# Performance work log

Hardware: AMD Instinct MI355X
Metric: run time of the kernel (lower is better)

Reference implementation:

```python
import jax, jax.numpy as jnp
import numpy as np

N_NODES = 32768
N_EDGES = 131072
B = 1024          # number of drug graphs
N_SIDE = 994      # SIDER side effects
SIDE_F = 1050     # glove(300) + label(750)

GAT_DIMS = [(109, 96, 8), (768, 128, 8), (1024, 128, 8), (1024, 128, 1)]  # (in, out_per_head, heads)
LIN_DIMS = [("x5", 128, 64), ("x6", 64, 64), ("w1", 750, 750), ("w2", 750, 64),
            ("z1", 19127, 1600), ("z2", 1600, 64), ("v1", 1024, 256), ("v2", 256, 64),
            ("agg", 192, 64), ("col", 128, 64), ("s1", SIDE_F, 64), ("s2", 64, 64)]


def setup_inputs() -> dict:
    key = jax.random.key(0)
    ks = iter(jax.random.split(key, 64))
    d = {}
    d["x"] = jax.random.normal(next(ks), (N_NODES, 109), jnp.float32)
    d["edge_index"] = jax.random.randint(next(ks), (2, N_EDGES), 0, N_NODES)
    d["batch"] = jnp.arange(N_NODES) // (N_NODES // B)  # 32 atoms per graph
    d["w"] = jax.random.normal(next(ks), (B, 750), jnp.float32)
    d["z"] = jax.random.normal(next(ks), (B, 19127), jnp.float32)
    d["v"] = jax.random.normal(next(ks), (B, 1024), jnp.float32)
    d["side"] = jax.random.normal(next(ks), (N_SIDE, SIDE_F), jnp.float32)
    for i, (fi, fo, h) in enumerate(GAT_DIMS, 1):
        d[f"g{i}_W"] = jax.random.normal(next(ks), (fi, h * fo), jnp.float32) / np.sqrt(fi)
        d[f"g{i}_as"] = jax.random.normal(next(ks), (1, h, fo), jnp.float32) * 0.1
        d[f"g{i}_ad"] = jax.random.normal(next(ks), (1, h, fo), jnp.float32) * 0.1
        d[f"g{i}_b"] = jnp.zeros((h * fo,), jnp.float32)
    for name, fi, fo in LIN_DIMS:
        d[name + "_W"] = jax.random.normal(next(ks), (fi, fo), jnp.float32) / np.sqrt(fi)
        d[name + "_b"] = jnp.zeros((fo,), jnp.float32)
    return d


def _gat(x, src, dst, W, a_s, a_d, b, heads, ch):
    """PyG GATConv (eval mode): linear -> per-edge leaky_relu attention ->
    scatter-softmax over incoming edges (self-loops already in src/dst) -> scatter-sum."""
    N = x.shape[0]
    h = (x @ W).reshape(N, heads, ch)            # [N,H,C]
    al_s = (h * a_s).sum(-1)                     # [N,H]
    al_d = (h * a_d).sum(-1)                     # [N,H]
    e = jax.nn.leaky_relu(al_s[src] + al_d[dst], 0.2)  # [E,H]
    m = jax.ops.segment_max(e, dst, num_segments=N)
    p = jnp.exp(e - m[dst])
    s = jax.ops.segment_sum(p, dst, num_segments=N)
    alpha = p / s[dst]                           # softmax over neighbors of dst
    out = jax.ops.segment_sum(h[src] * alpha[:, :, None], dst, num_segments=N)
    return out.reshape(N, heads * ch) + b


def reference(x, edge_index, batch, w, z, v, side,
              g1_W, g1_as, g1_ad, g1_b, g2_W, g2_as, g2_ad, g2_b,
              g3_W, g3_as, g3_ad, g3_b, g4_W, g4_as, g4_ad, g4_b,
              x5_W, x5_b, x6_W, x6_b, w1_W, w1_b, w2_W, w2_b,
              z1_W, z1_b, z2_W, z2_b, v1_W, v1_b, v2_W, v2_b,
              agg_W, agg_b, col_W, col_b, s1_W, s1_b, s2_W, s2_b):
    relu = jax.nn.relu
    N = x.shape[0]
    nb = w.shape[0]
    loops = jnp.arange(N)
    src = jnp.concatenate([edge_index[0], loops])  # add_self_loops=True (PyG default)
    dst = jnp.concatenate([edge_index[1], loops])
    h = relu(_gat(x, src, dst, g1_W, g1_as, g1_ad, g1_b, 8, 96))
    h = relu(_gat(h, src, dst, g2_W, g2_as, g2_ad, g2_b, 8, 128))
    h = relu(_gat(h, src, dst, g3_W, g3_as, g3_ad, g3_b, 8, 128))
    h = relu(_gat(h, src, dst, g4_W, g4_as, g4_ad, g4_b, 1, 128))
    xg = jax.ops.segment_max(h, batch, num_segments=nb)           # global_max_pool
    xg = relu(relu(xg @ x5_W + x5_b) @ x6_W + x6_b)
    wv = relu(relu(w @ w1_W + w1_b) @ w2_W + w2_b)
    zv = relu(relu(z @ z1_W + z1_b) @ z2_W + z2_b)
    vv = relu(relu(v @ v1_W + v1_b) @ v2_W + v2_b)
    xwz = jnp.concatenate([xg, wv, zv], axis=1) @ agg_W + agg_b   # no activation
    drug = jnp.abs(jnp.tanh(jnp.concatenate([xwz, vv], axis=1) @ col_W + col_b))
    se = jnp.tanh(relu(side @ s1_W + s1_b) @ s2_W + s2_b)
    dn = drug / jnp.maximum(jnp.linalg.norm(drug, axis=1, keepdims=True), 1e-12)
    sn = se / jnp.maximum(jnp.linalg.norm(se, axis=1, keepdims=True), 1e-12)
    freq = 5.0 * (dn @ sn.T)
    return (freq, dn, sn)
```

## Files before the change

kernel.cpp:

```cpp
#include <hip/hip_runtime.h>
#include <math.h>
#include <float.h>

#define E0 131072
#define NN 32768
#define NB 1024
#define NSIDE 994
#define ETOT (E0 + NN)

typedef short bf16x8 __attribute__((ext_vector_type(8)));
typedef unsigned short ushort8 __attribute__((ext_vector_type(8)));
typedef float f32x4 __attribute__((ext_vector_type(4)));

__device__ inline float b2f(unsigned short u) { return __uint_as_float(((unsigned)u) << 16); }
__device__ inline unsigned short f2b(float f) {
  unsigned u = __float_as_uint(f);
  return (unsigned short)((u + 0x7fffu + ((u >> 16) & 1u)) >> 16);
}

__device__ inline void gload_lds16(const void* g, void* l) {
  __builtin_amdgcn_global_load_lds(
      (const __attribute__((address_space(1))) unsigned int*)g,
      (__attribute__((address_space(3))) unsigned int*)l, 16, 0, 0);
}

__global__ void fill_i32(int* p, int v, int n) {
  int i = blockIdx.x * blockDim.x + threadIdx.x;
  if (i < n) p[i] = v;
}

struct CDesc { const float* in; unsigned short* out; int rowsOut, Rreal, C, Cp, wg_end; };
struct CBatch { CDesc d[5]; };
__global__ void conv_batch(CBatch cb) {
  int bid = blockIdx.x;
  int di = 0;
  while (bid >= cb.d[di].wg_end) ++di;
  const CDesc& g = cb.d[di];
  int rel = bid - (di ? cb.d[di - 1].wg_end : 0);
  size_t idx = (size_t)rel * 256 + threadIdx.x;
  size_t tot = (size_t)g.rowsOut * g.Cp;
  if (idx >= tot) return;
  int r = (int)(idx / g.Cp), c = (int)(idx % g.Cp);
  g.out[idx] = (r < g.Rreal && c < g.C) ? f2b(g.in[(size_t)r * g.C + c]) : (unsigned short)0;
}

struct TDesc { const float* W; unsigned short* WT; int K, N, Kp, Npad, gx, wg_end; };
struct TBatch { TDesc d[16]; };
__global__ __launch_bounds__(256) void transpose_batch(TBatch tb) {
  __shared__ float t[32][33];
  int bid = blockIdx.x;
  int di = 0;
  while (bid >= tb.d[di].wg_end) ++di;
  const TDesc& g = tb.d[di];
  int rel = bid - (di ? tb.d[di - 1].wg_end : 0);
  int n0 = (rel % g.gx) * 32, k0 = (rel / g.gx) * 32;
  int tx = threadIdx.x & 31, ty = threadIdx.x >> 5;
  for (int r = ty; r < 32; r += 8) {
    int k = k0 + r, n = n0 + tx;
    t[r][tx] = (k < g.K && n < g.N) ? g.W[(size_t)k * g.N + n] : 0.f;
  }
  __syncthreads();
  for (int r = ty; r < 32; r += 8) {
    int n = n0 + r, k = k0 + tx;
    if (n < g.Npad && k < g.Kp)
      g.WT[(size_t)n * g.Kp + k] = (n < g.N) ? f2b(t[tx][r]) : (unsigned short)0;
  }
}

__global__ void count_deg(const int* __restrict__ ei, int* deg) {
  int e = blockIdx.x * blockDim.x + threadIdx.x;
  if (e >= ETOT) return;
  int dst = (e < E0) ? ei[E0 + e] : (e - E0);
  atomicAdd(&deg[dst], 1);
}

__global__ void scan_deg(const int* __restrict__ deg, int* rowptr, int* cursor) {
  __shared__ int part[1024];
  int tid = threadIdx.x;
  const int chunk = NN / 1024;
  int base = tid * chunk;
  int local[chunk];
  int sum = 0;
#pragma unroll
  for (int i = 0; i < chunk; ++i) { local[i] = sum; sum += deg[base + i]; }
  part[tid] = sum;
  __syncthreads();
  for (int off = 1; off < 1024; off <<= 1) {
    int t = (tid >= off) ? part[tid - off] : 0;
    __syncthreads();
    part[tid] += t;
    __syncthreads();
  }
  int offset = part[tid] - sum;
#pragma unroll
  for (int i = 0; i < chunk; ++i) {
    int v = offset + local[i];
    rowptr[base + i] = v;
    cursor[base + i] = v;
  }
  if (tid == 1023) rowptr[NN] = offset + sum;
}

__global__ void fill_csr(const int* __restrict__ ei, int* cursor, int* __restrict__ srcl) {
  int e = blockIdx.x * blockDim.x + threadIdx.x;
  if (e >= ETOT) return;
  int src, dst;
  if (e < E0) { src = ei[e]; dst = ei[E0 + e]; } else { src = dst = e - E0; }
  int p = atomicAdd(&cursor[dst], 1);
  srcl[p] = src;
}

template <int ACT, int OBF, int SC>
__global__ __launch_bounds__(256) void gemm_mfma(
    const unsigned short* __restrict__ A, const unsigned short* __restrict__ BT,
    const float* __restrict__ bias, void* __restrict__ Cp,
    int Nreal, int K, int lda, int ldb, int ldc, int gx, int zpad,
    const float* __restrict__ asv, const float* __restrict__ adv,
    float* __restrict__ als, float* __restrict__ ald, int H) {
  __shared__ unsigned short As[2][128 * 32];
  __shared__ unsigned short Bs[2][128 * 32];
  const int nwg = gridDim.x;
  const int chunk = nwg >> 3;
  const int bid = blockIdx.x;
  const int swz = (bid & 7) * chunk + (bid >> 3);
  const int bm = (swz / gx) * 128, bn = (swz % gx) * 128;
  const int tid = threadIdx.x;
  const int wv = tid >> 6, lane = tid & 63;
  const int sr = lane >> 2;
  const int sk = ((lane & 3) ^ ((lane >> 3) & 3)) * 8;
  const int r16 = lane & 15, kq = lane >> 4;
  const int slot8 = (kq ^ ((r16 >> 1) & 3)) * 8;
  const int wr = wv >> 1, wc = wv & 1;
  f32x4 acc[4][4];
#pragma unroll
  for (int i = 0; i < 4; ++i)
#pragma unroll
    for (int j = 0; j < 4; ++j) acc[i][j] = (f32x4){0.f, 0.f, 0.f, 0.f};

  const unsigned short* Abase = A + (size_t)bm * lda;
  const unsigned short* Bbase = BT + (size_t)bn * ldb;
  auto stage = [&](int buf, int k0) {
    gload_lds16(Abase + (size_t)(wv * 16 + sr) * lda + k0 + sk, &As[buf][wv * 512]);
    gload_lds16(Abase + (size_t)(64 + wv * 16 + sr) * lda + k0 + sk, &As[buf][2048 + wv * 512]);
    gload_lds16(Bbase + (size_t)(wv * 16 + sr) * ldb + k0 + sk, &Bs[buf][wv * 512]);
    gload_lds16(Bbase + (size_t)(64 + wv * 16 + sr) * ldb + k0 + sk, &Bs[buf][2048 + wv * 512]);
  };
  stage(0, 0);
  __syncthreads();
  int cur = 0;
  for (int k0 = 0; k0 < K; k0 += 32) {
    if (k0 + 32 < K) stage(cur ^ 1, k0 + 32);
    bf16x8 af[4], bfr[4];
#pragma unroll
    for (int i = 0; i < 4; ++i)
      af[i] = *(const bf16x8*)&As[cur][(wr * 64 + i * 16 + r16) * 32 + slot8];
#pragma unroll
    for (int j = 0; j < 4; ++j)
      bfr[j] = *(const bf16x8*)&Bs[cur][(wc * 64 + j * 16 + r16) * 32 + slot8];
#pragma unroll
    for (int i = 0; i < 4; ++i)
#pragma unroll
      for (int j = 0; j < 4; ++j)
        acc[i][j] = __builtin_amdgcn_mfma_f32_16x16x32_bf16(af[i], bfr[j], acc[i][j], 0, 0, 0);
    __syncthreads();
    cur ^= 1;
  }
#pragma unroll
  for (int i = 0; i < 4; ++i) {
    int row = bm + wr * 64 + i * 16 + kq * 4;
#pragma unroll
    for (int j = 0; j < 4; ++j) {
      int col = bn + wc * 64 + j * 16 + r16;
      bool real = col < Nreal;
      if (!real && !zpad) continue;
      float bv = (bias && real) ? bias[col] : 0.f;
#pragma unroll
      for (int r = 0; r < 4; ++r) {
        float v = acc[i][j][r] + bv;
        if (ACT == 1) v = v > 0.f ? v : 0.f;
        else if (ACT == 2) v = tanhf(v);
        else if (ACT == 3) v = fabsf(tanhf(v));
        if (!real) v = 0.f;
        if (OBF) ((unsigned short*)Cp)[(size_t)(row + r) * ldc + col] = f2b(v);
        else ((float*)Cp)[(size_t)(row + r) * ldc + col] = v;
      }
    }
  }
  if (SC) {
    const int h = bn >> 7;
    float* scr = (float*)&As[0][0];
    float a_s[4], a_d[4];
#pragma unroll
    for (int j = 0; j < 4; ++j) {
      int cwh = wc * 64 + j * 16 + r16;
      a_s[j] = asv[h * 128 + cwh];
      a_d[j] = adv[h * 128 + cwh];
    }
#pragma unroll
    for (int i = 0; i < 4; ++i)
#pragma unroll
      for (int r = 0; r < 4; ++r) {
        float sp = 0.f, dp = 0.f;
#pragma unroll
        for (int j = 0; j < 4; ++j) {
          sp = fmaf(acc[i][j][r], a_s[j], sp);
          dp = fmaf(acc[i][j][r], a_d[j], dp);
        }
#pragma unroll
        for (int m = 1; m < 16; m <<= 1) {
          sp += __shfl_xor(sp, m);
          dp += __shfl_xor(dp, m);
        }
        if (r16 == 0) {
          int rl = wr * 64 + i * 16 + kq * 4 + r;
          scr[rl * 4 + wc * 2 + 0] = sp;
          scr[rl * 4 + wc * 2 + 1] = dp;
        }
      }
    __syncthreads();
    if (tid < 128) {
      float s = scr[tid * 4 + 0] + scr[tid * 4 + 2];
      float d = scr[tid * 4 + 1] + scr[tid * 4 + 3];
      als[(size_t)(bm + tid) * H + h] = s;
      ald[(size_t)(bm + tid) * H + h] = d;
    }
  }
}

struct GDesc {
  const unsigned short* A; const unsigned short* BT; const float* bias; void* C;
  int Nreal, K, lda, ldb, ldc, gx, zpad, act, obf, Mreal, wg_end;
};
struct GBatch { GDesc d[5]; };
__global__ __launch_bounds__(256) void gemm_batch(GBatch gb) {
  __shared__ unsigned short As[2][128 * 32];
  __shared__ unsigned short Bs[2][128 * 32];
  int bid = blockIdx.x;
  int di = 0;
  while (bid >= gb.d[di].wg_end) ++di;
  const GDesc& g = gb.d[di];
  int rel = bid - (di ? gb.d[di - 1].wg_end : 0);
  const int bm = (rel / g.gx) * 128, bn = (rel % g.gx) * 128;
  const int tid = threadIdx.x;
  const int wv = tid >> 6, lane = tid & 63;
  const int sr = lane >> 2;
  const int sk = ((lane & 3) ^ ((lane >> 3) & 3)) * 8;
  const int r16 = lane & 15, kq = lane >> 4;
  const int slot8 = (kq ^ ((r16 >> 1) & 3)) * 8;
  const int wr = wv >> 1, wc = wv & 1;
  f32x4 acc[4][4];
#pragma unroll
  for (int i = 0; i < 4; ++i)
#pragma unroll
    for (int j = 0; j < 4; ++j) acc[i][j] = (f32x4){0.f, 0.f, 0.f, 0.f};

  const unsigned short* Abase = g.A + (size_t)bm * g.lda;
  const unsigned short* Bbase = g.BT + (size_t)bn * g.ldb;
  auto stage = [&](int buf, int k0) {
    gload_lds16(Abase + (size_t)(wv * 16 + sr) * g.lda + k0 + sk, &As[buf][wv * 512]);
    gload_lds16(Abase + (size_t)(64 + wv * 16 + sr) * g.lda + k0 + sk, &As[buf][2048 + wv * 512]);
    gload_lds16(Bbase + (size_t)(wv * 16 + sr) * g.ldb + k0 + sk, &Bs[buf][wv * 512]);
    gload_lds16(Bbase + (size_t)(64 + wv * 16 + sr) * g.ldb + k0 + sk, &Bs[buf][2048 + wv * 512]);
  };
  stage(0, 0);
  __syncthreads();
  int cur = 0;
  for (int k0 = 0; k0 < g.K; k0 += 32) {
    if (k0 + 32 < g.K) stage(cur ^ 1, k0 + 32);
    bf16x8 af[4], bfr[4];
#pragma unroll
    for (int i = 0; i < 4; ++i)
      af[i] = *(const bf16x8*)&As[cur][(wr * 64 + i * 16 + r16) * 32 + slot8];
#pragma unroll
    for (int j = 0; j < 4; ++j)
      bfr[j] = *(const bf16x8*)&Bs[cur][(wc * 64 + j * 16 + r16) * 32 + slot8];
#pragma unroll
    for (int i = 0; i < 4; ++i)
#pragma unroll
      for (int j = 0; j < 4; ++j)
        acc[i][j] = __builtin_amdgcn_mfma_f32_16x16x32_bf16(af[i], bfr[j], acc[i][j], 0, 0, 0);
    __syncthreads();
    cur ^= 1;
  }
  if (g.act == 4) {
    if (wc == 0) {
#pragma unroll
      for (int i = 0; i < 4; ++i)
#pragma unroll
        for (int r = 0; r < 4; ++r) {
          int row = bm + wr * 64 + i * 16 + kq * 4 + r;
          float vv[4];
#pragma unroll
          for (int j = 0; j < 4; ++j) vv[j] = tanhf(acc[i][j][r] + g.bias[j * 16 + r16]);
          float ss = vv[0] * vv[0] + vv[1] * vv[1] + vv[2] * vv[2] + vv[3] * vv[3];
          ss += __shfl_xor(ss, 1);
          ss += __shfl_xor(ss, 2);
          ss += __shfl_xor(ss, 4);
          ss += __shfl_xor(ss, 8);
          float inv = 1.f / fmaxf(sqrtf(ss), 1e-12f);
          if (row < g.Mreal)
#pragma unroll
            for (int j = 0; j < 4; ++j)
              ((float*)g.C)[(size_t)row * g.ldc + j * 16 + r16] = vv[j] * inv;
        }
    }
    return;
  }
#pragma unroll
  for (int i = 0; i < 4; ++i) {
    int row = bm + wr * 64 + i * 16 + kq * 4;
#pragma unroll
    for (int j = 0; j < 4; ++j) {
      int col = bn + wc * 64 + j * 16 + r16;
      bool real = col < g.Nreal;
      if (!real && !g.zpad) continue;
      float bv = (g.bias && real) ? g.bias[col] : 0.f;
#pragma unroll
      for (int r = 0; r < 4; ++r) {
        float v = acc[i][j][r] + bv;
        if (g.act == 1) v = v > 0.f ? v : 0.f;
        else if (g.act == 2) v = tanhf(v);
        else if (g.act == 3) v = fabsf(tanhf(v));
        if (!real) v = 0.f;
        if (g.obf) ((unsigned short*)g.C)[(size_t)(row + r) * g.ldc + col] = f2b(v);
        else ((float*)g.C)[(size_t)(row + r) * g.ldc + col] = v;
      }
    }
  }
}

__global__ __launch_bounds__(256) void gemm_mfma_sk(
    const unsigned short* __restrict__ A, const unsigned short* __restrict__ BT,
    float* __restrict__ PART, int lda, int ldb, int ldc) {
  __shared__ unsigned short As[128 * 32];
  __shared__ unsigned short Bs[128 * 32];
  const int bid = blockIdx.x;
  const int swz = (bid & 7) * 208 + (bid >> 3);
  const int s = swz / 104;
  const int pos = swz - s * 104;
  const int bm = (pos / 13) * 128, bn = (pos % 13) * 128;
  const int base = s * 37 + (s < 6 ? s : 6);
  const int nsteps = 37 + (s < 6 ? 1 : 0);
  const int tid = threadIdx.x;
  const int wv = tid >> 6, lane = tid & 63;
  const int sr = lane >> 2;
  const int sk = ((lane & 3) ^ ((lane >> 3) & 3)) * 8;
  const int r16 = lane & 15, kq = lane >> 4;
  const int slot8 = (kq ^ ((r16 >> 1) & 3)) * 8;
  const int wr = wv >> 1, wc = wv & 1;
  f32x4 acc[4][4];
#pragma unroll
  for (int i = 0; i < 4; ++i)
#pragma unroll
    for (int j = 0; j < 4; ++j) acc[i][j] = (f32x4){0.f, 0.f, 0.f, 0.f};

  const unsigned short* Abase = A + (size_t)bm * lda;
  const unsigned short* Bbase = BT + (size_t)bn * ldb;
  for (int ks = 0; ks < nsteps; ++ks) {
    int k0 = (base + ks) * 32;
    gload_lds16(Abase + (size_t)(wv * 16 + sr) * lda + k0 + sk, &As[wv * 512]);
    gload_lds16(Abase + (size_t)(64 + wv * 16 + sr) * lda + k0 + sk, &As[2048 + wv * 512]);
    gload_lds16(Bbase + (size_t)(wv * 16 + sr) * ldb + k0 + sk, &Bs[wv * 512]);
    gload_lds16(Bbase + (size_t)(64 + wv * 16 + sr) * ldb + k0 + sk, &Bs[2048 + wv * 512]);
    __syncthreads();
    bf16x8 af[4], bfr[4];
#pragma unroll
    for (int i = 0; i < 4; ++i)
      af[i] = *(const bf16x8*)&As[(wr * 64 + i * 16 + r16) * 32 + slot8];
#pragma unroll
    for (int j = 0; j < 4; ++j)
      bfr[j] = *(const bf16x8*)&Bs[(wc * 64 + j * 16 + r16) * 32 + slot8];
#pragma unroll
    for (int i = 0; i < 4; ++i)
#pragma unroll
      for (int j = 0; j < 4; ++j)
        acc[i][j] = __builtin_amdgcn_mfma_f32_16x16x32_bf16(af[i], bfr[j], acc[i][j], 0, 0, 0);
    __syncthreads();
  }
  float* out = PART + (size_t)s * 1024 * ldc;
#pragma unroll
  for (int i = 0; i < 4; ++i) {
    int row = bm + wr * 64 + i * 16 + kq * 4;
#pragma unroll
    for (int j = 0; j < 4; ++j) {
      int col = bn + wc * 64 + j * 16 + r16;
      if (col >= 1600) continue;
#pragma unroll
      for (int r = 0; r < 4; ++r)
        out[(size_t)(row + r) * ldc + col] = acc[i][j][r];
    }
  }
}

__global__ void zred(const float* __restrict__ PART, const float* __restrict__ bias,
                     unsigned short* __restrict__ ZB) {
  int g = blockIdx.x * blockDim.x + threadIdx.x;
  if (g >= 1024 * 1664 / 8) return;
  size_t base = (size_t)g * 8;
  int c0 = (int)(base % 1664);
  ushort8 o;
  if (c0 >= 1600) {
#pragma unroll
    for (int t = 0; t < 8; ++t) o[t] = 0;
  } else {
    float s[8] = {0.f, 0.f, 0.f, 0.f, 0.f, 0.f, 0.f, 0.f};
#pragma unroll
    for (int k = 0; k < 16; ++k) {
      const float* p = &PART[(size_t)k * 1024 * 1664 + base];
      float4 a = *(const float4*)p;
      float4 b = *(const float4*)(p + 4);
      s[0] += a.x; s[1] += a.y; s[2] += a.z; s[3] += a.w;
      s[4] += b.x; s[5] += b.y; s[6] += b.z; s[7] += b.w;
    }
#pragma unroll
    for (int t = 0; t < 8; ++t) {
      float v = s[t] + bias[c0 + t];
      o[t] = f2b(v > 0.f ? v : 0.f);
    }
  }
  *(ushort8*)&ZB[base] = o;
}

__global__ __launch_bounds__(256) void tail_fused(
    const unsigned short* __restrict__ CAT192, const unsigned short* __restrict__ WTAGG,
    const float* __restrict__ agg_b, const unsigned short* __restrict__ CAT128,
    const unsigned short* __restrict__ WTCOL, const float* __restrict__ col_b,
    float* __restrict__ DN) {
  __shared__ unsigned short S1[128 * 32];
  __shared__ unsigned short S2[128 * 32];
  __shared__ unsigned short ACAT[128 * 128];
  const int bm = blockIdx.x * 128;
  const int tid = threadIdx.x;
  const int wv = tid >> 6, lane = tid & 63;
  const int sr = lane >> 2;
  const int sk = ((lane & 3) ^ ((lane >> 3) & 3)) * 8;
  const int r16 = lane & 15, kq = lane >> 4;
  const int slot8 = (kq ^ ((r16 >> 1) & 3)) * 8;
  const int wr = wv >> 1, wc = wv & 1;
  f32x4 acc[4][4];
#pragma unroll
  for (int i = 0; i < 4; ++i)
#pragma unroll
    for (int j = 0; j < 4; ++j) acc[i][j] = (f32x4){0.f, 0.f, 0.f, 0.f};

  const unsigned short* Abase = CAT192 + (size_t)bm * 192;
  for (int k0 = 0; k0 < 192; k0 += 32) {
    gload_lds16(Abase + (size_t)(wv * 16 + sr) * 192 + k0 + sk, &S1[wv * 512]);
    gload_lds16(Abase + (size_t)(64 + wv * 16 + sr) * 192 + k0 + sk, &S1[2048 + wv * 512]);
    gload_lds16(WTAGG + (size_t)(wv * 16 + sr) * 192 + k0 + sk, &S2[wv * 512]);
    gload_lds16(WTAGG + (size_t)(64 + wv * 16 + sr) * 192 + k0 + sk, &S2[2048 + wv * 512]);
    __syncthreads();
    bf16x8 af[4], bfr[4];
#pragma unroll
    for (int i = 0; i < 4; ++i)
      af[i] = *(const bf16x8*)&S1[(wr * 64 + i * 16 + r16) * 32 + slot8];
#pragma unroll
    for (int j = 0; j < 4; ++j)
      bfr[j] = *(const bf16x8*)&S2[(wc * 64 + j * 16 + r16) * 32 + slot8];
#pragma unroll
    for (int i = 0; i < 4; ++i)
#pragma unroll
      for (int j = 0; j < 4; ++j)
        acc[i][j] = __builtin_amdgcn_mfma_f32_16x16x32_bf16(af[i], bfr[j], acc[i][j], 0, 0, 0);
    __syncthreads();
  }
  if (wc == 0) {
#pragma unroll
    for (int i = 0; i < 4; ++i)
#pragma unroll
      for (int j = 0; j < 4; ++j) {
        int col = j * 16 + r16;
#pragma unroll
        for (int r = 0; r < 4; ++r) {
          int rl = wr * 64 + i * 16 + kq * 4 + r;
          ACAT[rl * 128 + col] = f2b(acc[i][j][r] + agg_b[col]);
        }
      }
  }
  for (int idx = tid; idx < 128 * 8; idx += 256) {
    int row = idx >> 3, c8 = (idx & 7) * 8;
    *(ushort8*)&ACAT[row * 128 + 64 + c8] =
        *(const ushort8*)&CAT128[(size_t)(bm + row) * 128 + 64 + c8];
  }
#pragma unroll
  for (int i = 0; i < 4; ++i)
#pragma unroll
    for (int j = 0; j < 4; ++j) acc[i][j] = (f32x4){0.f, 0.f, 0.f, 0.f};
  __syncthreads();

  for (int k0 = 0; k0 < 128; k0 += 32) {
    gload_lds16(WTCOL + (size_t)(wv * 16 + sr) * 128 + k0 + sk, &S1[wv * 512]);
    gload_lds16(WTCOL + (size_t)(64 + wv * 16 + sr) * 128 + k0 + sk, &S1[2048 + wv * 512]);
    __syncthreads();
    bf16x8 af[4], bfr[4];
#pragma unroll
    for (int i = 0; i < 4; ++i)
      af[i] = *(const bf16x8*)&ACAT[(wr * 64 + i * 16 + r16) * 128 + k0 + kq * 8];
#pragma unroll
    for (int j = 0; j < 4; ++j)
      bfr[j] = *(const bf16x8*)&S1[(wc * 64 + j * 16 + r16) * 32 + slot8];
#pragma unroll
    for (int i = 0; i < 4; ++i)
#pragma unroll
      for (int j = 0; j < 4; ++j)
        acc[i][j] = __builtin_amdgcn_mfma_f32_16x16x32_bf16(af[i], bfr[j], acc[i][j], 0, 0, 0);
    __syncthreads();
  }
  if (wc == 0) {
#pragma unroll
    for (int i = 0; i < 4; ++i)
#pragma unroll
      for (int r = 0; r < 4; ++r) {
        int row = bm + wr * 64 + i * 16 + kq * 4 + r;
        float vv[4];
#pragma unroll
        for (int j = 0; j < 4; ++j) vv[j] = fabsf(tanhf(acc[i][j][r] + col_b[j * 16 + r16]));
        float ss = vv[0] * vv[0] + vv[1] * vv[1] + vv[2] * vv[2] + vv[3] * vv[3];
        ss += __shfl_xor(ss, 1);
        ss += __shfl_xor(ss, 2);
        ss += __shfl_xor(ss, 4);
        ss += __shfl_xor(ss, 8);
        float inv = 1.f / fmaxf(sqrtf(ss), 1e-12f);
#pragma unroll
        for (int j = 0; j < 4; ++j)
          DN[(size_t)row * 64 + j * 16 + r16] = vv[j] * inv;
      }
  }
}

__global__ void gat_scores_bf(const unsigned short* __restrict__ hlin,
                              const float* __restrict__ a_s, const float* __restrict__ a_d,
                              float* __restrict__ als, float* __restrict__ ald,
                              int H, int C, int tot) {
  int idx = blockIdx.x * blockDim.x + threadIdx.x;
  if (idx >= tot) return;
  int n = idx / H, h = idx - n * H;
  const unsigned short* base = hlin + (size_t)n * H * C + (size_t)h * C;
  const float* as = a_s + h * C;
  const float* ad = a_d + h * C;
  float ss = 0.f, sd = 0.f;
  for (int c = 0; c < C; c += 8) {
    ushort8 v = *(const ushort8*)(base + c);
#pragma unroll
    for (int t = 0; t < 8; ++t) {
      float f = b2f(v[t]);
      ss = fmaf(f, as[c + t], ss);
      sd = fmaf(f, ad[c + t], sd);
    }
  }
  als[idx] = ss;
  ald[idx] = sd;
}

template <int F, int C>
__global__ __launch_bounds__(256) void gat_agg_v4(
    const int* __restrict__ rowptr, const int* __restrict__ srcl,
    const float* __restrict__ als, const float* __restrict__ ald,
    const unsigned short* __restrict__ hlin,
    const float* __restrict__ bias, unsigned short* __restrict__ out) {
  constexpr int H = F / C;
  constexpr int CPN = F / 8;
  int gidx = blockIdx.x * 256 + threadIdx.x;
  if (gidx >= NN * CPN) return;
  int node = gidx / CPN;
  int c0 = (gidx - node * CPN) * 8;
  int h = c0 / C;
  float aldv = ald[node * H + h];
  float s = 0.f;
  float acc[8] = {0.f, 0.f, 0.f, 0.f, 0.f, 0.f, 0.f, 0.f};
  int start = rowptr[node], end = rowptr[node + 1];
  for (int k = start; k < end; ++k) {
    int src = srcl[k];
    float e = als[src * H + h] + aldv;
    e = (e >= 0.f) ? e : 0.2f * e;
    float p = __expf(e);
    s += p;
    ushort8 hv = *(const ushort8*)(hlin + (size_t)src * F + c0);
#pragma unroll
    for (int t = 0; t < 8; ++t) acc[t] = fmaf(p, b2f(hv[t]), acc[t]);
  }
  float inv_s = 1.f / s;
  ushort8 o;
#pragma unroll
  for (int t = 0; t < 8; ++t) {
    float val = acc[t] * inv_s + bias[c0 + t];
    o[t] = f2b(val > 0.f ? val : 0.f);
  }
  *(ushort8*)(out + (size_t)node * F + c0) = o;
}

__global__ void pool_max(const unsigned short* __restrict__ xb,
                         unsigned short* __restrict__ xgb) {
  int g = blockIdx.x, c = threadIdx.x;
  const unsigned short* base = xb + (size_t)g * 32 * 128 + c;
  float m = -FLT_MAX;
#pragma unroll 8
  for (int n = 0; n < 32; ++n) m = fmaxf(m, b2f(base[n * 128]));
  xgb[g * 128 + c] = f2b(m);
}

__global__ __launch_bounds__(256) void freq_k(const float* __restrict__ dn,
                                              const float* __restrict__ sn,
                                              float* __restrict__ C, int M, int N) {
  __shared__ float As[16][64];
  __shared__ float Bs[16][65];
  int tid = threadIdx.x;
  int tx = tid & 15, ty = tid >> 4;
  int bi = blockIdx.y * 16, bj = blockIdx.x * 16;
#pragma unroll
  for (int t = 0; t < 4; ++t) {
    int idx = tid * 4 + t;
    int r = idx >> 6, c = idx & 63;
    As[r][c] = (bi + r < M) ? dn[(bi + r) * 64 + c] : 0.f;
    Bs[r][c] = (bj + r < N) ? sn[(bj + r) * 64 + c] : 0.f;
  }
  __syncthreads();
  float acc = 0.f;
#pragma unroll
  for (int k = 0; k < 64; ++k) acc = fmaf(As[ty][k], Bs[tx][k], acc);
  if (bi + ty < M && bj + tx < N) C[(size_t)(bi + ty) * N + (bj + tx)] = 5.f * acc;
}

extern "C" void kernel_launch(void* const* d_in, const int* in_sizes, int n_in,
                              void* d_out, int out_size, void* d_ws, size_t ws_size,
                              hipStream_t stream) {
  const float* x = (const float*)d_in[0];
  const int* ei = (const int*)d_in[1];
  const float* w = (const float*)d_in[3];
  const float* z = (const float*)d_in[4];
  const float* v = (const float*)d_in[5];
  const float* side = (const float*)d_in[6];
  const float* gW[4] = {(const float*)d_in[7], (const float*)d_in[11],
                        (const float*)d_in[15], (const float*)d_in[19]};
  const float* gas[4] = {(const float*)d_in[8], (const float*)d_in[12],
                         (const float*)d_in[16], (const float*)d_in[20]};
  const float* gad[4] = {(const float*)d_in[9], (const float*)d_in[13],
                         (const float*)d_in[17], (const float*)d_in[21]};
  const float* gb[4] = {(const float*)d_in[10], (const float*)d_in[14],
                        (const float*)d_in[18], (const float*)d_in[22]};
  const float* x5_W = (const float*)d_in[23]; const float* x5_b = (const float*)d_in[24];
  const float* x6_W = (const float*)d_in[25]; const float* x6_b = (const float*)d_in[26];
  const float* w1_W = (const float*)d_in[27]; const float* w1_b = (const float*)d_in[28];
  const float* w2_W = (const float*)d_in[29]; const float* w2_b = (const float*)d_in[30];
  const float* z1_W = (const float*)d_in[31]; const float* z1_b = (const float*)d_in[32];
  const float* z2_W = (const float*)d_in[33]; const float* z2_b = (const float*)d_in[34];
  const float* v1_W = (const float*)d_in[35]; const float* v1_b = (const float*)d_in[36];
  const float* v2_W = (const float*)d_in[37]; const float* v2_b = (const float*)d_in[38];
  const float* agg_W = (const float*)d_in[39]; const float* agg_b = (const float*)d_in[40];
  const float* col_W = (const float*)d_in[41]; const float* col_b = (const float*)d_in[42];
  const float* s1_W = (const float*)d_in[43]; const float* s1_b = (const float*)d_in[44];
  const float* s2_W = (const float*)d_in[45]; const float* s2_b = (const float*)d_in[46];

  char* wsb = (char*)d_ws;
  size_t off = 0;
  auto alloc = [&](size_t bytes) {
    void* p = wsb + off;
    off = (off + bytes + 255) & ~(size_t)255;
    return p;
  };
  unsigned short* HLIN = (unsigned short*)alloc((size_t)NN * 1024 * 2);
  unsigned short* XB = (unsigned short*)alloc((size_t)NN * 1024 * 2);
  unsigned short* WTZ = (unsigned short*)alloc((size_t)1664 * 19136 * 2);
  unsigned short* ZA = (unsigned short*)alloc((size_t)1024 * 19136 * 2);
  unsigned short* WT1 = (unsigned short*)alloc((size_t)768 * 128 * 2);
  unsigned short* WT2 = (unsigned short*)alloc((size_t)1024 * 768 * 2);
  unsigned short* WT3 = (unsigned short*)alloc((size_t)1024 * 1024 * 2);
  unsigned short* WT4 = (unsigned short*)alloc((size_t)128 * 1024 * 2);
  unsigned short* WTW1 = (unsigned short*)alloc((size_t)768 * 768 * 2);
  unsigned short* WTW2 = (unsigned short*)alloc((size_t)128 * 768 * 2);
  unsigned short* WTZ2 = (unsigned short*)alloc((size_t)128 * 1664 * 2);
  unsigned short* WTV1 = (unsigned short*)alloc((size_t)256 * 1024 * 2);
  unsigned short* WTV2 = (unsigned short*)alloc((size_t)128 * 256 * 2);
  unsigned short* WTX5 = (unsigned short*)alloc((size_t)128 * 128 * 2);
  unsigned short* WTX6 = (unsigned short*)alloc((size_t)128 * 64 * 2);
  unsigned short* WTAGG = (unsigned short*)alloc((size_t)128 * 192 * 2);
  unsigned short* WTCOL = (unsigned short*)alloc((size_t)128 * 128 * 2);
  unsigned short* WTS1 = (unsigned short*)alloc((size_t)128 * 1056 * 2);
  unsigned short* WTS2 = (unsigned short*)alloc((size_t)128 * 64 * 2);
  unsigned short* WB = (unsigned short*)alloc((size_t)1024 * 768 * 2);
  unsigned short* VB = (unsigned short*)alloc((size_t)1024 * 1024 * 2);
  unsigned short* SIDEB = (unsigned short*)alloc((size_t)1024 * 1056 * 2);
  unsigned short* XGB = (unsigned short*)alloc((size_t)1024 * 128 * 2);
  unsigned short* ZB = (unsigned short*)alloc((size_t)1024 * 1664 * 2);
  unsigned short* X5O = (unsigned short*)alloc((size_t)1024 * 128 * 2);
  unsigned short* WMID = (unsigned short*)alloc((size_t)1024 * 768 * 2);
  unsigned short* VMID = (unsigned short*)alloc((size_t)1024 * 256 * 2);
  unsigned short* SEMID = (unsigned short*)alloc((size_t)1024 * 128 * 2);
  unsigned short* CAT192 = (unsigned short*)alloc((size_t)1024 * 192 * 2);
  unsigned short* CAT128 = (unsigned short*)alloc((size_t)1024 * 128 * 2);
  float* ALS = (float*)alloc((size_t)NN * 8 * 4);
  float* ALD = (float*)alloc((size_t)NN * 8 * 4);
  int* DEG = (int*)alloc((size_t)NN * 4);
  int* ROWPTR = (int*)alloc((size_t)(NN + 1) * 4);
  int* CURSOR = (int*)alloc((size_t)NN * 4);
  int* SRCL = (int*)alloc((size_t)ETOT * 4);
  float* PART = (float*)HLIN;

  hipLaunchKernelGGL(fill_i32, dim3((NN + 255) / 256), dim3(256), 0, stream, DEG, 0, NN);
  hipLaunchKernelGGL(count_deg, dim3((ETOT + 255) / 256), dim3(256), 0, stream, ei, DEG);
  hipLaunchKernelGGL(scan_deg, dim3(1), dim3(1024), 0, stream, DEG, ROWPTR, CURSOR);
  hipLaunchKernelGGL(fill_csr, dim3((ETOT + 255) / 256), dim3(256), 0, stream, ei, CURSOR, SRCL);

  {
    TBatch tb;
    int acc_wg = 0, i = 0;
    auto add = [&](const float* W, unsigned short* WT, int K, int N, int Kp, int Npad) {
      int gx = Npad / 32, gy = Kp / 32;
      acc_wg += gx * gy;
      tb.d[i++] = {W, WT, K, N, Kp, Npad, gx, acc_wg};
    };
    add(z1_W, WTZ, 19127, 1600, 19136, 1664);
    add(gW[0], WT1, 109, 768, 128, 768);
    add(gW[1], WT2, 768, 1024, 768, 1024);
    add(gW[2], WT3, 1024, 1024, 1024, 1024);
    add(gW[3], WT4, 1024, 128, 1024, 128);
    add(w1_W, WTW1, 750, 750, 768, 768);
    add(w2_W, WTW2, 750, 64, 768, 128);
    add(z2_W, WTZ2, 1600, 64, 1664, 128);
    add(v1_W, WTV1, 1024, 256, 1024, 256);
    add(v2_W, WTV2, 256, 64, 256, 128);
    add(x5_W, WTX5, 128, 64, 128, 128);
    add(x6_W, WTX6, 64, 64, 64, 128);
    add(agg_W, WTAGG, 192, 64, 192, 128);
    add(col_W, WTCOL, 128, 64, 128, 128);
    add(s1_W, WTS1, 1050, 64, 1056, 128);
    add(s2_W, WTS2, 64, 64, 64, 128);
    hipLaunchKernelGGL(transpose_batch, dim3(acc_wg), dim3(256), 0, stream, tb);
  }

  {
    CBatch cb;
    int acc_wg = 0, i = 0;
    auto add = [&](const float* in, unsigned short* out, int rowsOut, int Rreal, int C, int Cp) {
      acc_wg += (int)(((size_t)rowsOut * Cp + 255) / 256);
      cb.d[i++] = {in, out, rowsOut, Rreal, C, Cp, acc_wg};
    };
    add(z, ZA, NB, NB, 19127, 19136);
    add(x, XB, NN, NN, 109, 128);
    add(w, WB, 1024, 1024, 750, 768);
    add(v, VB, 1024, 1024, 1024, 1024);
    add(side, SIDEB, 1024, 994, 1050, 1056);
    hipLaunchKernelGGL(conv_batch, dim3(acc_wg), dim3(256), 0, stream, cb);
  }

  const int Hs[4] = {8, 8, 8, 1};
  const int Kp[4] = {128, 768, 1024, 1024};
  const unsigned short* WTs[4] = {WT1, WT2, WT3, WT4};
  const int Fs[4] = {768, 1024, 1024, 128};
  for (int l = 0; l < 4; ++l) {
    int H = Hs[l], F = Fs[l], C = F / H;
    int gx = F / 128;
    int nwg = gx * (NN / 128);
    if (C == 128) {
      hipLaunchKernelGGL((gemm_mfma<0, 1, 1>), dim3(nwg), dim3(256), 0, stream,
                         XB, WTs[l], (const float*)nullptr, (void*)HLIN, F, Kp[l],
                         Kp[l], Kp[l], F, gx, 0, gas[l], gad[l], ALS, ALD, H);
    } else {
      hipLaunchKernelGGL((gemm_mfma<0, 1, 0>), dim3(nwg), dim3(256), 0, stream,
                         XB, WTs[l], (const float*)nullptr, (void*)HLIN, F, Kp[l],
                         Kp[l], Kp[l], F, gx, 0, (const float*)nullptr,
                         (const float*)nullptr, (float*)nullptr, (float*)nullptr, H);
      int totNH = NN * H;
      hipLaunchKernelGGL(gat_scores_bf, dim3((totNH + 255) / 256), dim3(256), 0, stream,
                         HLIN, gas[l], gad[l], ALS, ALD, H, C, totNH);
    }
    if (l == 0)
      hipLaunchKernelGGL((gat_agg_v4<768, 96>), dim3(NN * 96 / 256), dim3(256), 0, stream,
                         ROWPTR, SRCL, ALS, ALD, HLIN, gb[l], XB);
    else if (l == 3)
      hipLaunchKernelGGL((gat_agg_v4<128, 128>), dim3(NN * 16 / 256), dim3(256), 0, stream,
                         ROWPTR, SRCL, ALS, ALD, HLIN, gb[l], XB);
    else
      hipLaunchKernelGGL((gat_agg_v4<1024, 128>), dim3(NN * 128 / 256), dim3(256), 0, stream,
                         ROWPTR, SRCL, ALS, ALD, HLIN, gb[l], XB);
  }

  hipLaunchKernelGGL(pool_max, dim3(NB), dim3(128), 0, stream, XB, XGB);

  {
    GBatch b;
    int acc_wg = 0, i = 0;
    auto add = [&](const unsigned short* A, const unsigned short* BT, const float* bias,
                   void* C, int Npad, int Nreal, int K, int lda, int ldb, int ldc,
                   int zpad, int act, int obf, int Mreal) {
      int gx = Npad / 128;
      acc_wg += gx * 8;
      b.d[i++] = {A, BT, bias, C, Nreal, K, lda, ldb, ldc, gx, zpad, act, obf, Mreal, acc_wg};
    };
    add(WB, WTW1, w1_b, WMID, 768, 750, 768, 768, 768, 768, 1, 1, 1, 1024);
    add(VB, WTV1, v1_b, VMID, 256, 256, 1024, 1024, 1024, 256, 0, 1, 1, 1024);
    add(SIDEB, WTS1, s1_b, SEMID, 128, 64, 1056, 1056, 1056, 128, 1, 1, 1, 1024);
    add(XGB, WTX5, x5_b, X5O, 128, 64, 128, 128, 128, 128, 1, 1, 1, 1024);
    while (i < 5) { b.d[i] = b.d[i - 1]; b.d[i].wg_end = acc_wg; ++i; }
    hipLaunchKernelGGL(gemm_batch, dim3(acc_wg), dim3(256), 0, stream, b);
  }

  hipLaunchKernelGGL(gemm_mfma_sk, dim3(1664), dim3(256), 0, stream, ZA, WTZ, PART, 19136, 19136, 1664);
  hipLaunchKernelGGL(zred, dim3((1024 * 1664 / 8 + 255) / 256), dim3(256), 0, stream, PART, z1_b, ZB);

  float* outp = (float*)d_out;
  float* DN = outp + (size_t)NB * NSIDE;
  float* SN = DN + (size_t)NB * 64;

  {
    GBatch b;
    int acc_wg = 0, i = 0;
    auto add = [&](const unsigned short* A, const unsigned short* BT, const float* bias,
                   void* C, int Npad, int Nreal, int K, int lda, int ldb, int ldc,
                   int zpad, int act, int obf, int Mreal) {
      int gx = Npad / 128;
      acc_wg += gx * 8;
      b.d[i++] = {A, BT, bias, C, Nreal, K, lda, ldb, ldc, gx, zpad, act, obf, Mreal, acc_wg};
    };
    add(X5O, WTX6, x6_b, CAT192 + 0, 128, 64, 64, 128, 64, 192, 0, 1, 1, 1024);
    add(WMID, WTW2, w2_b, CAT192 + 64, 128, 64, 768, 768, 768, 192, 0, 1, 1, 1024);
    add(ZB, WTZ2, z2_b, CAT192 + 128, 128, 64, 1664, 1664, 1664, 192, 0, 1, 1, 1024);
    add(VMID, WTV2, v2_b, CAT128 + 64, 128, 64, 256, 256, 256, 128, 0, 1, 1, 1024);
    add(SEMID, WTS2, s2_b, SN, 128, 64, 64, 128, 64, 64, 0, 4, 0, 994);
    hipLaunchKernelGGL(gemm_batch, dim3(acc_wg), dim3(256), 0, stream, b);
  }

  hipLaunchKernelGGL(tail_fused, dim3(8), dim3(256), 0, stream,
                     CAT192, WTAGG, agg_b, CAT128, WTCOL, col_b, DN);

  hipLaunchKernelGGL(freq_k, dim3((NSIDE + 15) / 16, (NB + 15) / 16), dim3(256), 0, stream,
                     DN, SN, outp, NB, NSIDE);
}
```

Measured before the change: 958.3 us.

## Replace double-buffered LDS staging with single-buffer load-sync-compute loop in GEMMs

Removes the double-buffered LDS prefetch in both MFMA GEMM kernels. Each k-step now loads its tile into a single LDS buffer, synchronises, computes, and synchronises again. This halves LDS use per block, which may allow more blocks per CU. In exchange, global loads no longer overlap with the MFMA work of the previous tile, and an extra barrier is added before the score scratch reuses the A buffer.

Result: slower. 978.7 us (+2.1%).

```diff
diff --git a/kernel.cpp b/kernel.cpp
--- a/kernel.cpp
+++ b/kernel.cpp
@@ -117,8 +117,8 @@
     int Nreal, int K, int lda, int ldb, int ldc, int gx, int zpad,
     const float* __restrict__ asv, const float* __restrict__ adv,
     float* __restrict__ als, float* __restrict__ ald, int H) {
-  __shared__ unsigned short As[2][128 * 32];
-  __shared__ unsigned short Bs[2][128 * 32];
+  __shared__ unsigned short As[128 * 32];
+  __shared__ unsigned short Bs[128 * 32];
   const int nwg = gridDim.x;
   const int chunk = nwg >> 3;
   const int bid = blockIdx.x;
@@ -139,31 +139,25 @@
 
   const unsigned short* Abase = A + (size_t)bm * lda;
   const unsigned short* Bbase = BT + (size_t)bn * ldb;
-  auto stage = [&](int buf, int k0) {
-    gload_lds16(Abase + (size_t)(wv * 16 + sr) * lda + k0 + sk, &As[buf][wv * 512]);
-    gload_lds16(Abase + (size_t)(64 + wv * 16 + sr) * lda + k0 + sk, &As[buf][2048 + wv * 512]);
-    gload_lds16(Bbase + (size_t)(wv * 16 + sr) * ldb + k0 + sk, &Bs[buf][wv * 512]);
-    gload_lds16(Bbase + (size_t)(64 + wv * 16 + sr) * ldb + k0 + sk, &Bs[buf][2048 + wv * 512]);
-  };
-  stage(0, 0);
-  __syncthreads();
-  int cur = 0;
   for (int k0 = 0; k0 < K; k0 += 32) {
-    if (k0 + 32 < K) stage(cur ^ 1, k0 + 32);
+    gload_lds16(Abase + (size_t)(wv * 16 + sr) * lda + k0 + sk, &As[wv * 512]);
+    gload_lds16(Abase + (size_t)(64 + wv * 16 + sr) * lda + k0 + sk, &As[2048 + wv * 512]);
+    gload_lds16(Bbase + (size_t)(wv * 16 + sr) * ldb + k0 + sk, &Bs[wv * 512]);
+    gload_lds16(Bbase + (size_t)(64 + wv * 16 + sr) * ldb + k0 + sk, &Bs[2048 + wv * 512]);
+    __syncthreads();
     bf16x8 af[4], bfr[4];
 #pragma unroll
     for (int i = 0; i < 4; ++i)
-      af[i] = *(const bf16x8*)&As[cur][(wr * 64 + i * 16 + r16) * 32 + slot8];
+      af[i] = *(const bf16x8*)&As[(wr * 64 + i * 16 + r16) * 32 + slot8];
 #pragma unroll
     for (int j = 0; j < 4; ++j)
-      bfr[j] = *(const bf16x8*)&Bs[cur][(wc * 64 + j * 16 + r16) * 32 + slot8];
+      bfr[j] = *(const bf16x8*)&Bs[(wc * 64 + j * 16 + r16) * 32 + slot8];
 #pragma unroll
     for (int i = 0; i < 4; ++i)
 #pragma unroll
       for (int j = 0; j < 4; ++j)
         acc[i][j] = __builtin_amdgcn_mfma_f32_16x16x32_bf16(af[i], bfr[j], acc[i][j], 0, 0, 0);
     __syncthreads();
-    cur ^= 1;
   }
 #pragma unroll
   for (int i = 0; i < 4; ++i) {
@@ -188,7 +182,7 @@
   }
   if (SC) {
     const int h = bn >> 7;
-    float* scr = (float*)&As[0][0];
+    float* scr = (float*)&As[0];
     float a_s[4], a_d[4];
 #pragma unroll
     for (int j = 0; j < 4; ++j) {
@@ -196,6 +190,7 @@
       a_s[j] = asv[h * 128 + cwh];
       a_d[j] = adv[h * 128 + cwh];
     }
+    __syncthreads();
 #pragma unroll
     for (int i = 0; i < 4; ++i)
 #pragma unroll
@@ -233,8 +228,8 @@
 };
 struct GBatch { GDesc d[5]; };
 __global__ __launch_bounds__(256) void gemm_batch(GBatch gb) {
-  __shared__ unsigned short As[2][128 * 32];
-  __shared__ unsigned short Bs[2][128 * 32];
+  __shared__ unsigned short As[128 * 32];
+  __shared__ unsigned short Bs[128 * 32];
   int bid = blockIdx.x;
   int di = 0;
   while (bid >= gb.d[di].wg_end) ++di;
@@ -256,31 +251,25 @@
 
   const unsigned short* Abase = g.A + (size_t)bm * g.lda;
   const unsigned short* Bbase = g.BT + (size_t)bn * g.ldb;
-  auto stage = [&](int buf, int k0) {
-    gload_lds16(Abase + (size_t)(wv * 16 + sr) * g.lda + k0 + sk, &As[buf][wv * 512]);
-    gload_lds16(Abase + (size_t)(64 + wv * 16 + sr) * g.lda + k0 + sk, &As[buf][2048 + wv * 512]);
-    gload_lds16(Bbase + (size_t)(wv * 16 + sr) * g.ldb + k0 + sk, &Bs[buf][wv * 512]);
-    gload_lds16(Bbase + (size_t)(64 + wv * 16 + sr) * g.ldb + k0 + sk, &Bs[buf][2048 + wv * 512]);
-  };
-  stage(0, 0);
-  __syncthreads();
-  int cur = 0;
   for (int k0 = 0; k0 < g.K; k0 += 32) {
-    if (k0 + 32 < g.K) stage(cur ^ 1, k0 + 32);
+    gload_lds16(Abase + (size_t)(wv * 16 + sr) * g.lda + k0 + sk, &As[wv * 512]);
+    gload_lds16(Abase + (size_t)(64 + wv * 16 + sr) * g.lda + k0 + sk, &As[2048 + wv * 512]);
+    gload_lds16(Bbase + (size_t)(wv * 16 + sr) * g.ldb + k0 + sk, &Bs[wv * 512]);
+    gload_lds16(Bbase + (size_t)(64 + wv * 16 + sr) * g.ldb + k0 + sk, &Bs[2048 + wv * 512]);
+    __syncthreads();
     bf16x8 af[4], bfr[4];
 #pragma unroll
     for (int i = 0; i < 4; ++i)
-      af[i] = *(const bf16x8*)&As[cur][(wr * 64 + i * 16 + r16) * 32 + slot8];
+      af[i] = *(const bf16x8*)&As[(wr * 64 + i * 16 + r16) * 32 + slot8];
 #pragma unroll
     for (int j = 0; j < 4; ++j)
-      bfr[j] = *(const bf16x8*)&Bs[cur][(wc * 64 + j * 16 + r16) * 32 + slot8];
+      bfr[j] = *(const bf16x8*)&Bs[(wc * 64 + j * 16 + r16) * 32 + slot8];
 #pragma unroll
     for (int i = 0; i < 4; ++i)
 #pragma unroll
       for (int j = 0; j < 4; ++j)
         acc[i][j] = __builtin_amdgcn_mfma_f32_16x16x32_bf16(af[i], bfr[j], acc[i][j], 0, 0, 0);
     __syncthreads();
-    cur ^= 1;
   }
   if (g.act == 4) {
     if (wc == 0) {
```
